# Kernel optimization log

Hardware: AMD Instinct MI355X
Metric: run time of the kernel (lower is better)

Reference implementation:

```python
import jax, jax.numpy as jnp
import numpy as np
from jax import lax

A = 20          # alphabet size (input_size)
L = 512         # max_seq_length
CH = 8          # conv channels
N_LAYERS = 9    # log2(512) conv+pool stages


def setup_inputs() -> dict:
    key = jax.random.key(0)
    ks = jax.random.split(key, 6)
    B = 1024
    idx = jax.random.randint(ks[0], (B, L), 0, A)
    lens = jax.random.randint(ks[1], (B,), L // 4, L + 1)
    masks = jnp.arange(L)[None, :] < lens[:, None]            # [B, L] bool
    # one-hot sequences, zeroed at padded positions (so nonzero() skips them)
    x = jax.nn.one_hot(idx, A, dtype=jnp.float32) * masks[..., None].astype(jnp.float32)
    blosum = jax.random.normal(ks[2], (A, A), jnp.float32)
    blosum = (blosum + blosum.T) * 0.5                        # symmetric like BLOSUM
    lpm = blosum                                              # trainable copy
    pm = jnp.clip(blosum, 0.0)                                # clamp(min=0) constant
    std = jnp.ones((1,), jnp.float32)                         # Gaussian std for row decay
    w0 = jax.random.normal(ks[3], (CH, 1, 3), jnp.float32) * 0.3
    ws = jax.random.normal(ks[4], (N_LAYERS - 1, CH, CH, 3), jnp.float32) * 0.2
    return {"x": x, "masks": masks, "lpm": lpm, "pm": pm, "std": std, "w0": w0, "ws": ws}


def _shift_pos(m, k):
    # target index clamp(s + k, max=L-1): shift right by k, boundary index L-1
    # collects any source in the last k+1 positions (set semantics -> OR).
    head = jnp.zeros(m.shape[:-1] + (k,), dtype=bool)
    body = m[..., : L - k - 1]                                # targets k .. L-2
    last = jnp.any(m[..., L - 1 - k:], axis=-1, keepdims=True)
    return jnp.concatenate([head, body, last], axis=-1)


def _shift_neg(m, k):
    # target index clamp(s - k, min=0)
    first = jnp.any(m[..., : k + 1], axis=-1, keepdims=True)
    body = m[..., k + 1:]                                     # targets 1 .. L-1-k
    tail = jnp.zeros(m.shape[:-1] + (k,), dtype=bool)
    return jnp.concatenate([first, body, tail], axis=-1)


def _column(nz, lpm, pm):
    # Banded substitution scatter: each one-hot row i writes V[i, r] into row r
    # at the same (batch, seq) position. Original nested index_put loops collapse
    # to a single 20x20 matrix V applied via einsum (one-hot => no collisions).
    ii = jnp.arange(A)[:, None]
    rr = jnp.arange(A)[None, :]
    M = jnp.clip(lpm, 0.001, 1.0) * pm
    # up-writes: j in 1..18-i => i < r <= 18 ; down-writes: j in 1..i => r < i
    V = jnp.where((rr > ii) & (rr <= A - 2), M, 0.0) + jnp.where(rr < ii, M.T, 0.0)
    return jnp.einsum('bis,ir->brs', nz, V)


def _row(m, std):
    # Gaussian positional decay: writes exp(-k^2/(2 std^2)) at seq offsets +-k,
    # k = 1,2,3 in order (later k overwrites earlier at clamp collisions).
    row = jnp.zeros(m.shape, jnp.float32)
    for k in (1, 2, 3):
        mk = _shift_pos(m, k) | _shift_neg(m, k)
        vk = jnp.exp(-(k * k) / (2.0 * std * std))[0]
        row = jnp.where(mk, vk, row)
    return row


def _conv1d(h, w):
    # Conv1d(kernel=3, stride=1, pad=1, no bias)
    return lax.conv_general_dilated(h, w, (1,), [(1, 1)],
                                    dimension_numbers=('NCH', 'OIH', 'NCH'))


def _avgpool2(h):
    N, C, Lh = h.shape
    return h.reshape(N, C, Lh // 2, 2).mean(-1)


def reference(x, masks, lpm, pm, std, w0, ws):
    B = x.shape[0]
    xp = jnp.transpose(x, (0, 2, 1))          # [B, 20, L]
    m = xp != 0
    nz = m.astype(xp.dtype)
    h = xp + _column(nz, lpm, pm) + _row(m, std)
    h = h.reshape(B * A, 1, L)
    h = _avgpool2(_conv1d(h, w0))
    for i in range(N_LAYERS - 1):
        h = _avgpool2(_conv1d(h, ws[i]))
    return h.squeeze(-1).reshape(B, A, -1)    # [B, 20, 8]
```

## Files before the change

### kernel.cpp

```cpp
#include <hip/hip_runtime.h>
#include <math.h>

#define LSEQ 512
#define NA 20
#define NCH 8

__global__ __launch_bounds__(256) void wf_vt_kernel(
    const float* __restrict__ w0,
    const float* __restrict__ wsg,
    const float* __restrict__ lpm,
    const float* __restrict__ pm,
    float* __restrict__ wf,
    float* __restrict__ vtn)
{
    const int t = threadIdx.x;

    if (blockIdx.x == NCH) {
        for (int o = t; o < NA * NA; o += 256) {
            int j = o / NA, a = o % NA;
            float v = 0.f;
            if (a > j && a <= NA - 2)
                v += fminf(fmaxf(lpm[j * NA + a], 0.001f), 1.0f) * pm[j * NA + a];
            if (a < j)
                v += fminf(fmaxf(lpm[a * NA + j], 0.001f), 1.0f) * pm[a * NA + j];
            vtn[o] = v;
        }
        return;
    }

    const int r = blockIdx.x;

    __shared__ float gA[NCH * 256];
    __shared__ float gB[NCH * 256];
    __shared__ float4 s_e[NCH * NCH];

    if (t < NCH) gA[t * 256] = (t == r) ? 1.f : 0.f;
    __syncthreads();

    int P = 1;
    for (int step = 0; step < 8; ++step) {
        const int li = 7 - step;
        if (t < 64) {
            const int co = t >> 3, ci = t & 7;
            const float* wp = wsg + li * 192 + co * 24 + ci * 3;
            const float a0 = wp[0], a1 = wp[1], a2 = wp[2];
            s_e[co * 8 + ci] = make_float4(a0 + a1, a2, a1 + a2, a0);
        }
        __syncthreads();
        const float* gi = (step & 1) ? gB : gA;
        float* go = (step & 1) ? gA : gB;
        for (int it = t; it < NCH * P; it += 256) {
            const int ci = it >> step;
            const int p = it & (P - 1);
            float accE = 0.f, accO = 0.f;
#pragma unroll
            for (int co = 0; co < NCH; ++co) {
                const float g0 = gi[co * 256 + p];
                const float gm = (p > 0) ? gi[co * 256 + p - 1] : 0.f;
                const float gp = (p + 1 < P) ? gi[co * 256 + p + 1] : 0.f;
                const float4 e = s_e[co * 8 + ci];
                accE += e.x * g0 + e.y * gm;
                accO += e.z * g0 + e.w * gp;
            }
            *(float2*)(go + ci * 256 + 2 * p) = make_float2(0.5f * accE, 0.5f * accO);
        }
        __syncthreads();
        P <<= 1;
    }

    {
        const int p = t;
        float accE = 0.f, accO = 0.f;
#pragma unroll
        for (int co = 0; co < NCH; ++co) {
            const float g0 = gA[co * 256 + p];
            const float gm = (p > 0) ? gA[co * 256 + p - 1] : 0.f;
            const float gp = (p < 255) ? gA[co * 256 + p + 1] : 0.f;
            const float q0 = w0[co * 3 + 0], q1 = w0[co * 3 + 1], q2 = w0[co * 3 + 2];
            accE += (q0 + q1) * g0 + q2 * gm;
            accO += (q1 + q2) * g0 + q0 * gp;
        }
        *(float2*)(wf + r * 512 + 2 * p) = make_float2(0.5f * accE, 0.5f * accO);
    }
}

__global__ __launch_bounds__(256, 4) void main_kernel(
    const float* __restrict__ x,
    const float* __restrict__ vtn,
    const float* __restrict__ g_std,
    const float* __restrict__ wf,
    float* __restrict__ out)
{
    const int b = blockIdx.x;
    const int t = threadIdx.x;
    const int c = t & 7;
    const int seg = t >> 3;
    const int w = t >> 6;
    const int lane = t & 63;

    __shared__ __align__(16) float s_h[NA * 256];
    __shared__ __align__(16) float s_vtn[NA * NA];
    __shared__ float s_part[4 * NA * NCH];
    __shared__ unsigned char s_idx[LSEQ];

    const float* wbase = wf + c * 512 + seg * 4;
    const float4 wr0 = *(const float4*)(wbase + 0);
    const float4 wr1 = *(const float4*)(wbase + 128);
    const float4 wr2 = *(const float4*)(wbase + 256);
    const float4 wr3 = *(const float4*)(wbase + 384);

    if (t < NA * NA / 4) ((float4*)s_vtn)[t] = ((const float4*)vtn)[t];

    for (int i = t; i < 4 * NA * NCH; i += 256) s_part[i] = 0.f;

    const float4* xb = (const float4*)(x + (size_t)b * LSEQ * NA);
#pragma unroll
    for (int rep = 0; rep < 2; ++rep) {
        int s = t + rep * 256;
        int id = 255;
#pragma unroll
        for (int q = 0; q < 5; ++q) {
            float4 v = xb[s * 5 + q];
            if (v.x > .5f) id = 4 * q + 0;
            if (v.y > .5f) id = 4 * q + 1;
            if (v.z > .5f) id = 4 * q + 2;
            if (v.w > .5f) id = 4 * q + 3;
        }
        s_idx[s] = (unsigned char)id;
    }
    __syncthreads();

    const float stdv = g_std[0];
    const float inv2s2 = 1.f / (2.f * stdv * stdv);
    const float vks[3] = {__expf(-1.f * inv2s2), __expf(-4.f * inv2s2), __expf(-9.f * inv2s2)};

#pragma unroll
    for (int half = 0; half < 2; ++half) {
        {
            const int s = 256 * half + t;
            const int ai = s_idx[s];
            const bool valid = ai < NA;
#pragma unroll
            for (int a = 0; a < NA; ++a) {
                float v = valid ? (s_vtn[ai * NA + a] + (a == ai ? 1.f : 0.f)) : 0.f;
                s_h[a * 256 + t] = v;
            }
#pragma unroll
            for (int k = 1; k <= 3; ++k) {
                const float add = vks[k - 1];
                if (s == LSEQ - 1) {
                    for (int u = LSEQ - 1 - k; u <= LSEQ - 1; ++u) {
                        int tg = s_idx[u];
                        if (tg < NA)
                            s_h[tg * 256 + t] =
                                (valid ? s_vtn[ai * NA + tg] + (tg == ai ? 1.f : 0.f) : 0.f) + add;
                    }
                } else if (s >= k) {
                    int tg = s_idx[s - k];
                    if (tg < NA)
                        s_h[tg * 256 + t] =
                            (valid ? s_vtn[ai * NA + tg] + (tg == ai ? 1.f : 0.f) : 0.f) + add;
                }
                if (s == 0) {
                    for (int u = 0; u <= k; ++u) {
                        int tg = s_idx[u];
                        if (tg < NA)
                            s_h[tg * 256 + t] =
                                (valid ? s_vtn[ai * NA + tg] + (tg == ai ? 1.f : 0.f) : 0.f) + add;
                    }
                } else if (s + k < LSEQ) {
                    int tg = s_idx[s + k];
                    if (tg < NA)
                        s_h[tg * 256 + t] =
                            (valid ? s_vtn[ai * NA + tg] + (tg == ai ? 1.f : 0.f) : 0.f) + add;
                }
            }
        }
        __syncthreads();

        const float4 wA = half ? wr2 : wr0;
        const float4 wB = half ? wr3 : wr1;
#pragma unroll 1
        for (int a = 0; a < NA; ++a) {
            const float* hb = s_h + a * 256 + seg * 4;
            float4 h0 = *(const float4*)(hb);
            float4 h1 = *(const float4*)(hb + 128);
            float acc = h0.x * wA.x + h0.y * wA.y + h0.z * wA.z + h0.w * wA.w
                      + h1.x * wB.x + h1.y * wB.y + h1.z * wB.z + h1.w * wB.w;
            acc += __shfl_xor(acc, 8);
            acc += __shfl_xor(acc, 16);
            acc += __shfl_xor(acc, 32);
            if ((lane >> 3) == 0) s_part[w * (NA * NCH) + a * NCH + c] += acc;
        }
        __syncthreads();
    }

    if (t < NA * NCH)
        out[(size_t)b * (NA * NCH) + t] =
            s_part[t] + s_part[160 + t] + s_part[320 + t] + s_part[480 + t];
}

extern "C" void kernel_launch(void* const* d_in, const int* in_sizes, int n_in,
                              void* d_out, int out_size, void* d_ws, size_t ws_size,
                              hipStream_t stream) {
    const float* x    = (const float*)d_in[0];
    const float* lpm  = (const float*)d_in[2];
    const float* pm   = (const float*)d_in[3];
    const float* stdp = (const float*)d_in[4];
    const float* w0   = (const float*)d_in[5];
    const float* wsg  = (const float*)d_in[6];
    float* out = (float*)d_out;

    const int B = in_sizes[0] / (LSEQ * NA);

    float* vtn = (float*)d_ws;
    float* wfb = (float*)d_ws + 1024;

    wf_vt_kernel<<<dim3(NCH + 1), dim3(256), 0, stream>>>(w0, wsg, lpm, pm, wfb, vtn);
    main_kernel<<<dim3(B), dim3(256), 0, stream>>>(x, vtn, stdp, wfb, out);
}
```

Measured before the change: 111.1 us.

## Compute per-(alphabet,channel) dot products per thread instead of shuffle reductions

Replaces the warp-split dot product, which used shuffle reductions and partial sums in shared memory, with one thread per (a,c) output that serially dots its 256-element s_h row against the fused weight row read from global memory/cache. It also pads s_h rows to 260 and s_vtn rows to 33 to reduce LDS bank conflicts. This removes the shuffles, the s_part buffer and the final 4-way sum. In exchange only 160 of 256 threads work during the reduction, and each of them does a long serial loop with weight loads from global memory instead of registers.

```diff
diff --git a/kernel.cpp b/kernel.cpp
--- a/kernel.cpp
+++ b/kernel.cpp
@@ -4,6 +4,8 @@
 #define LSEQ 512
 #define NA 20
 #define NCH 8
+#define SH 260
+#define SV 33
 
 __global__ __launch_bounds__(256) void wf_vt_kernel(
     const float* __restrict__ w0,
@@ -93,25 +95,15 @@
 {
     const int b = blockIdx.x;
     const int t = threadIdx.x;
-    const int c = t & 7;
-    const int seg = t >> 3;
-    const int w = t >> 6;
-    const int lane = t & 63;
-
-    __shared__ __align__(16) float s_h[NA * 256];
-    __shared__ __align__(16) float s_vtn[NA * NA];
-    __shared__ float s_part[4 * NA * NCH];
+
+    __shared__ __align__(16) float s_h[NA * SH];
+    __shared__ float s_vtn[NA * SV];
     __shared__ unsigned char s_idx[LSEQ];
 
-    const float* wbase = wf + c * 512 + seg * 4;
-    const float4 wr0 = *(const float4*)(wbase + 0);
-    const float4 wr1 = *(const float4*)(wbase + 128);
-    const float4 wr2 = *(const float4*)(wbase + 256);
-    const float4 wr3 = *(const float4*)(wbase + 384);
-
-    if (t < NA * NA / 4) ((float4*)s_vtn)[t] = ((const float4*)vtn)[t];
-
-    for (int i = t; i < 4 * NA * NCH; i += 256) s_part[i] = 0.f;
+    for (int i = t; i < NA * NA; i += 256) {
+        int j = i / NA, a2 = i % NA;
+        s_vtn[j * SV + a2] = vtn[i];
+    }
 
     const float4* xb = (const float4*)(x + (size_t)b * LSEQ * NA);
 #pragma unroll
@@ -134,7 +126,8 @@
     const float inv2s2 = 1.f / (2.f * stdv * stdv);
     const float vks[3] = {__expf(-1.f * inv2s2), __expf(-4.f * inv2s2), __expf(-9.f * inv2s2)};
 
-#pragma unroll
+    float accT = 0.f;
+
     for (int half = 0; half < 2; ++half) {
         {
             const int s = 256 * half + t;
@@ -142,8 +135,8 @@
             const bool valid = ai < NA;
 #pragma unroll
             for (int a = 0; a < NA; ++a) {
-                float v = valid ? (s_vtn[ai * NA + a] + (a == ai ? 1.f : 0.f)) : 0.f;
-                s_h[a * 256 + t] = v;
+                float v = valid ? (s_vtn[ai * SV + a] + (a == ai ? 1.f : 0.f)) : 0.f;
+                s_h[a * SH + t] = v;
             }
 #pragma unroll
             for (int k = 1; k <= 3; ++k) {
@@ -152,52 +145,54 @@
                     for (int u = LSEQ - 1 - k; u <= LSEQ - 1; ++u) {
                         int tg = s_idx[u];
                         if (tg < NA)
-                            s_h[tg * 256 + t] =
-                                (valid ? s_vtn[ai * NA + tg] + (tg == ai ? 1.f : 0.f) : 0.f) + add;
+                            s_h[tg * SH + t] =
+                                (valid ? s_vtn[ai * SV + tg] + (tg == ai ? 1.f : 0.f) : 0.f) + add;
                     }
                 } else if (s >= k) {
                     int tg = s_idx[s - k];
                     if (tg < NA)
-                        s_h[tg * 256 + t] =
-                            (valid ? s_vtn[ai * NA + tg] + (tg == ai ? 1.f : 0.f) : 0.f) + add;
+                        s_h[tg * SH + t] =
+                            (valid ? s_vtn[ai * SV + tg] + (tg == ai ? 1.f : 0.f) : 0.f) + add;
                 }
                 if (s == 0) {
                     for (int u = 0; u <= k; ++u) {
                         int tg = s_idx[u];
                         if (tg < NA)
-                            s_h[tg * 256 + t] =
-                                (valid ? s_vtn[ai * NA + tg] + (tg == ai ? 1.f : 0.f) : 0.f) + add;
+                            s_h[tg * SH + t] =
+                                (valid ? s_vtn[ai * SV + tg] + (tg == ai ? 1.f : 0.f) : 0.f) + add;
                     }
                 } else if (s + k < LSEQ) {
                     int tg = s_idx[s + k];
                     if (tg < NA)
-                        s_h[tg * 256 + t] =
-                            (valid ? s_vtn[ai * NA + tg] + (tg == ai ? 1.f : 0.f) : 0.f) + add;
+                        s_h[tg * SH + t] =
+                            (valid ? s_vtn[ai * SV + tg] + (tg == ai ? 1.f : 0.f) : 0.f) + add;
                 }
             }
         }
         __syncthreads();
 
-        const float4 wA = half ? wr2 : wr0;
-        const float4 wB = half ? wr3 : wr1;
-#pragma unroll 1
-        for (int a = 0; a < NA; ++a) {
-            const float* hb = s_h + a * 256 + seg * 4;
-            float4 h0 = *(const float4*)(hb);
-            float4 h1 = *(const float4*)(hb + 128);
-            float acc = h0.x * wA.x + h0.y * wA.y + h0.z * wA.z + h0.w * wA.w
-                      + h1.x * wB.x + h1.y * wB.y + h1.z * wB.z + h1.w * wB.w;
-            acc += __shfl_xor(acc, 8);
-            acc += __shfl_xor(acc, 16);
-            acc += __shfl_xor(acc, 32);
-            if ((lane >> 3) == 0) s_part[w * (NA * NCH) + a * NCH + c] += acc;
+        if (t < NA * NCH) {
+            const int a = t >> 3;
+            const int c = t & 7;
+            const float* hr = s_h + a * SH;
+            const float* wr_ = wf + c * 512 + half * 256;
+            float acc0 = 0.f, acc1 = 0.f;
+#pragma unroll 4
+            for (int j = 0; j < 64; j += 2) {
+                float4 h0 = *(const float4*)(hr + 4 * j);
+                float4 w0v = *(const float4*)(wr_ + 4 * j);
+                float4 h1 = *(const float4*)(hr + 4 * j + 4);
+                float4 w1v = *(const float4*)(wr_ + 4 * j + 4);
+                acc0 += h0.x * w0v.x + h0.y * w0v.y + h0.z * w0v.z + h0.w * w0v.w;
+                acc1 += h1.x * w1v.x + h1.y * w1v.y + h1.z * w1v.z + h1.w * w1v.w;
+            }
+            accT += acc0 + acc1;
         }
         __syncthreads();
     }
 
     if (t < NA * NCH)
-        out[(size_t)b * (NA * NCH) + t] =
-            s_part[t] + s_part[160 + t] + s_part[320 + t] + s_part[480 + t];
+        out[(size_t)b * (NA * NCH) + t] = accT;
 }
 
 extern "C" void kernel_launch(void* const* d_in, const int* in_sizes, int n_in,
```

Measured after the change: 134.9 us. 1.21x slower.
